# Optimization experiments

Measured on AMD Instinct MI355X. Metric: run time of the kernel, lower is better.

Reference implementation:

```python
import jax, jax.numpy as jnp
import numpy as np

I = 128   # input_size
H = 256   # state_size


def setup_inputs() -> dict:
    key = jax.random.key(0)
    ks = jax.random.split(key, 7)
    T, B = 512, 1024
    # Xavier-ish init scales for params
    s_ih = 1.0 / np.sqrt(I)
    s_hh = 1.0 / np.sqrt(H)
    return {
        "x":    jax.random.normal(ks[0], (T, B, I), dtype=jnp.float32),
        "W_ih": jax.random.normal(ks[1], (4 * H, I), dtype=jnp.float32) * s_ih,
        "W_hh": jax.random.normal(ks[2], (4 * H, H), dtype=jnp.float32) * s_hh,
        "b_ih": jax.random.normal(ks[3], (4 * H,), dtype=jnp.float32) * s_hh,
        "b_hh": jax.random.normal(ks[4], (4 * H,), dtype=jnp.float32) * s_hh,
        "hx0":  jax.random.normal(ks[5], (H,), dtype=jnp.float32) * s_hh,
        "cx0":  jax.random.normal(ks[6], (H,), dtype=jnp.float32) * s_hh,
    }


def _lstm_forward(x, W_ih, W_hh, b_ih, b_hh, hx0, cx0):
    T, B, _ = x.shape
    past_length = T - 1  # use_last_past=False
    x_used = x[:past_length]
    # Precompute input projections for all steps at once: [T-1, B, 4H]
    x_proj = jnp.einsum("tbi,gi->tbg", x_used, W_ih) + b_ih + b_hh

    h0 = jnp.broadcast_to(hx0, (B, H))
    c0 = jnp.broadcast_to(cx0, (B, H))

    def step(carry, xp):
        h, c = carry
        gates = xp + h @ W_hh.T  # [B, 4H]
        i_g, f_g, g_g, o_g = jnp.split(gates, 4, axis=-1)
        i_g = jax.nn.sigmoid(i_g)
        f_g = jax.nn.sigmoid(f_g)
        g_g = jnp.tanh(g_g)
        o_g = jax.nn.sigmoid(o_g)
        c_new = f_g * c + i_g * g_g
        h_new = o_g * jnp.tanh(c_new)
        return (h_new, c_new), None

    (h, c), _ = jax.lax.scan(step, (h0, c0), x_proj)
    return h, c


def reference(x, W_ih, W_hh, b_ih, b_hh, hx0, cx0):
    return _lstm_forward(x, W_ih, W_hh, b_ih, b_hh, hx0, cx0)
```

## Files before the change

kernel.cpp:

```cpp
#include <hip/hip_runtime.h>
#include <hip/hip_bf16.h>


#define T_STEPS 511
#define BATCH   1024
#define IN      128
#define HID     256
#define NG      1024
#define KTOT    384
#define BWG     16
#define NGROUP  64
#define SW      264
#define HS      264

typedef __bf16 bf16x8 __attribute__((ext_vector_type(8)));
typedef float  f32x4  __attribute__((ext_vector_type(4)));
typedef unsigned long long u64;

#define WCAT_OFF 0
#define BIAS_OFF 786432
#define HEXG_OFF 790528
#define CNT_OFF  1839104

__global__ void precast_kernel(const float* __restrict__ W_ih,
                               const float* __restrict__ W_hh,
                               const float* __restrict__ b_ih,
                               const float* __restrict__ b_hh,
                               __bf16* __restrict__ wcat,
                               float* __restrict__ bias,
                               int* __restrict__ cnt) {
    int idx = blockIdx.x * blockDim.x + threadIdx.x;
    if (idx < NG * KTOT) {
        int n = idx / KTOT, k = idx % KTOT;
        float v = (k < IN) ? W_ih[n * IN + k] : W_hh[n * HID + (k - IN)];
        wcat[idx] = (__bf16)v;
    }
    if (idx < NG) bias[idx] = b_ih[idx] + b_hh[idx];
    if (idx < NGROUP * 32) cnt[idx] = 0;
}

__device__ __forceinline__ float sigmoidf_fast(float v) {
    return 1.f / (1.f + __expf(-v));
}
__device__ __forceinline__ float tanhf_fast(float v) {
    return 1.f - 2.f / (1.f + __expf(2.f * v));
}

#define MFMA(a, b, c) __builtin_amdgcn_mfma_f32_16x16x32_bf16((a), (b), (c), 0, 0, 0)

__device__ __forceinline__ bf16x8 cvt_pack(float4 lo, float4 hi) {
    return bf16x8{(__bf16)lo.x, (__bf16)lo.y, (__bf16)lo.z, (__bf16)lo.w,
                  (__bf16)hi.x, (__bf16)hi.y, (__bf16)hi.z, (__bf16)hi.w};
}

__global__ __launch_bounds__(512, 2) void lstm_kernel(
    const float* __restrict__ x,
    const __bf16* __restrict__ wcat,
    const float* __restrict__ bias,
    const float* __restrict__ hx0,
    const float* __restrict__ cx0,
    __bf16* __restrict__ hexg,
    int* __restrict__ cnt,
    float* __restrict__ out)
{
    __shared__ alignas(16) __bf16 Whh[256 * SW];
    __shared__ alignas(16) __bf16 Ah[BWG * HS];

    const int tid  = threadIdx.x;
    const int bx   = blockIdx.x;
    const int g    = bx & 63;
    const int s    = bx >> 6;
    const int wave = tid >> 6;
    const int lane = tid & 63;
    const int col  = lane & 15;
    const int quad = lane >> 4;
    const int hf   = col >> 3;
    const int b0   = g * BWG;
    const int j0   = s * 64;
    const int jcol = j0 + wave * 8 + (col & 7);

    int* cntg = cnt + g * 32;

    {
        int r  = tid >> 1;
        int hh = (tid & 1) * 128;
        int ngl = ((r >> 6) << 8) + j0 + (r & 63);
        const __bf16* src = wcat + (size_t)ngl * KTOT + IN + hh;
        __bf16* dst = &Whh[r * SW + hh];
        #pragma unroll
        for (int i = 0; i < 16; ++i)
            *(bf16x8*)(dst + i * 8) = *(const bf16x8*)(src + i * 8);
    }

    const int n0 = (hf ? 256 : 0) + jcol;
    const int n1 = 512 + (hf ? 256 : 0) + jcol;
    bf16x8 wi0[4], wi1[4];
    #pragma unroll
    for (int ks = 0; ks < 4; ++ks) {
        wi0[ks] = *(const bf16x8*)(wcat + (size_t)n0 * KTOT + ks * 32 + quad * 8);
        wi1[ks] = *(const bf16x8*)(wcat + (size_t)n1 * KTOT + ks * 32 + quad * 8);
    }

    const float bi  = bias[jcol];
    const float bfv = bias[256 + jcol];
    const float bg  = bias[512 + jcol];
    const float bo  = bias[768 + jcol];

    float cst[4], hn[4];
    {
        float cv = cx0[jcol];
        #pragma unroll
        for (int r = 0; r < 4; ++r) cst[r] = cv;
    }

    float4 x0f[8], xf[8];
    #pragma unroll
    for (int ks = 0; ks < 4; ++ks) {
        const float* xp = x + (size_t)(b0 + col) * IN + ks * 32 + quad * 8;
        x0f[2 * ks]     = *(const float4*)xp;
        x0f[2 * ks + 1] = *(const float4*)(xp + 4);
        const float* xq = xp + (size_t)BATCH * IN;
        xf[2 * ks]      = *(const float4*)xq;
        xf[2 * ks + 1]  = *(const float4*)(xq + 4);
    }

    const int nl0 = hf * 64 + wave * 8 + (col & 7);
    const __bf16* wl0 = &Whh[nl0 * SW + quad * 8];
    const __bf16* wl1 = &Whh[(128 + nl0) * SW + quad * 8];

    __syncthreads();

    f32x4 aA0 = {0.f,0.f,0.f,0.f}, aA1 = {0.f,0.f,0.f,0.f};
    f32x4 aB0 = {0.f,0.f,0.f,0.f}, aB1 = {0.f,0.f,0.f,0.f};
    {
        bf16x8 ax[4];
        #pragma unroll
        for (int ks = 0; ks < 4; ++ks)
            ax[ks] = cvt_pack(x0f[2 * ks], x0f[2 * ks + 1]);
        aA0 = MFMA(ax[0], wi0[0], aA0); aB0 = MFMA(ax[0], wi1[0], aB0);
        aA1 = MFMA(ax[1], wi0[1], aA1); aB1 = MFMA(ax[1], wi1[1], aB1);
        aA0 = MFMA(ax[2], wi0[2], aA0); aB0 = MFMA(ax[2], wi1[2], aB0);
        aA1 = MFMA(ax[3], wi0[3], aA1); aB1 = MFMA(ax[3], wi1[3], aB1);
    }

    for (int t = 0; t < T_STEPS; ++t) {
        bf16x8 ahf[8];
        if (t == 0) {
            #pragma unroll
            for (int ks = 0; ks < 8; ++ks) {
                const float* hp = hx0 + ks * 32 + quad * 8;
                ahf[ks] = cvt_pack(*(const float4*)hp, *(const float4*)(hp + 4));
            }
        } else {
            const int target = 32 * t;
            int guard = 0;
            while (__hip_atomic_load(cntg, __ATOMIC_RELAXED,
                                     __HIP_MEMORY_SCOPE_AGENT) < target) {
                __builtin_amdgcn_s_sleep(1);
                if (++guard > (1 << 22)) break;
            }
            const u64* sp = (const u64*)(hexg
                + ((size_t)((t & 1) * NGROUP + g)) * (BWG * HID)) + tid * 2;
            u64 v0 = __hip_atomic_load(sp,     __ATOMIC_RELAXED, __HIP_MEMORY_SCOPE_AGENT);
            u64 v1 = __hip_atomic_load(sp + 1, __ATOMIC_RELAXED, __HIP_MEMORY_SCOPE_AGENT);
            int row = tid >> 5, c8 = (tid & 31) * 8;
            *(u64*)&Ah[row * HS + c8]     = v0;
            *(u64*)&Ah[row * HS + c8 + 4] = v1;
            __syncthreads();
            #pragma unroll
            for (int ks = 0; ks < 8; ++ks)
                ahf[ks] = *(const bf16x8*)&Ah[col * HS + ks * 32 + quad * 8];
        }

        #pragma unroll
        for (int ks = 0; ks < 4; ++ks) {
            bf16x8 w0a = *(const bf16x8*)(wl0 + ks * 32);
            bf16x8 w1a = *(const bf16x8*)(wl1 + ks * 32);
            bf16x8 w0b = *(const bf16x8*)(wl0 + (ks + 4) * 32);
            bf16x8 w1b = *(const bf16x8*)(wl1 + (ks + 4) * 32);
            aA0 = MFMA(ahf[ks],     w0a, aA0);
            aB0 = MFMA(ahf[ks],     w1a, aB0);
            aA1 = MFMA(ahf[ks + 4], w0b, aA1);
            aB1 = MFMA(ahf[ks + 4], w1b, aB1);
        }
        f32x4 accA = aA0 + aA1;
        f32x4 accB = aB0 + aB1;

        #pragma unroll
        for (int r = 0; r < 4; ++r) {
            float oA = __shfl_xor(accA[r], 8, 64);
            float oB = __shfl_xor(accB[r], 8, 64);
            float iv = (hf ? oA : accA[r]) + bi;
            float fv = (hf ? accA[r] : oA) + bfv;
            float gv = (hf ? oB : accB[r]) + bg;
            float ov = (hf ? accB[r] : oB) + bo;
            float ig = sigmoidf_fast(iv);
            float fg = sigmoidf_fast(fv);
            float gt = tanhf_fast(gv);
            float og = sigmoidf_fast(ov);
            float cn = fg * cst[r] + ig * gt;
            cst[r] = cn;
            hn[r]  = og * tanhf_fast(cn);
        }

        if (t < T_STEPS - 1) {
            __bf16* base = hexg
                + ((size_t)((((t + 1) & 1) * NGROUP) + g)) * (BWG * HID);
            #pragma unroll
            for (int r = 0; r < 4; ++r) {
                unsigned short mine;
                {
                    __bf16 hv = (__bf16)hn[r];
                    __builtin_memcpy(&mine, &hv, 2);
                }
                int other = __shfl_xor((int)mine, 1, 64);
                if ((col & 1) == 0 && col < 8) {
                    unsigned int val = (unsigned int)mine
                                     | ((unsigned int)(unsigned short)other << 16);
                    unsigned int* p = (unsigned int*)(base
                        + (size_t)(quad * 4 + r) * HID + jcol);
                    __hip_atomic_store(p, val, __ATOMIC_RELAXED,
                                       __HIP_MEMORY_SCOPE_AGENT);
                }
            }
            asm volatile("s_waitcnt vmcnt(0)" ::: "memory");
            if (lane == 0)
                __hip_atomic_fetch_add(cntg, 1, __ATOMIC_RELAXED,
                                       __HIP_MEMORY_SCOPE_AGENT);

            {
                bf16x8 ax[4];
                #pragma unroll
                for (int ks = 0; ks < 4; ++ks)
                    ax[ks] = cvt_pack(xf[2 * ks], xf[2 * ks + 1]);
                aA0 = {0.f,0.f,0.f,0.f}; aA1 = {0.f,0.f,0.f,0.f};
                aB0 = {0.f,0.f,0.f,0.f}; aB1 = {0.f,0.f,0.f,0.f};
                aA0 = MFMA(ax[0], wi0[0], aA0); aB0 = MFMA(ax[0], wi1[0], aB0);
                aA1 = MFMA(ax[1], wi0[1], aA1); aB1 = MFMA(ax[1], wi1[1], aB1);
                aA0 = MFMA(ax[2], wi0[2], aA0); aB0 = MFMA(ax[2], wi1[2], aB0);
                aA1 = MFMA(ax[3], wi0[3], aA1); aB1 = MFMA(ax[3], wi1[3], aB1);
            }
            if (t + 2 <= T_STEPS - 1) {
                #pragma unroll
                for (int ks = 0; ks < 4; ++ks) {
                    const float* xp = x + (size_t)(t + 2) * BATCH * IN
                                    + (size_t)(b0 + col) * IN + ks * 32 + quad * 8;
                    xf[2 * ks]     = *(const float4*)xp;
                    xf[2 * ks + 1] = *(const float4*)(xp + 4);
                }
            }
        }
    }

    if (col < 8) {
        #pragma unroll
        for (int r = 0; r < 4; ++r) {
            int row = b0 + quad * 4 + r;
            out[(size_t)row * HID + jcol] = hn[r];
            out[(size_t)BATCH * HID + (size_t)row * HID + jcol] = cst[r];
        }
    }
}

extern "C" void kernel_launch(void* const* d_in, const int* in_sizes, int n_in,
                              void* d_out, int out_size, void* d_ws, size_t ws_size,
                              hipStream_t stream) {
    const float* x    = (const float*)d_in[0];
    const float* W_ih = (const float*)d_in[1];
    const float* W_hh = (const float*)d_in[2];
    const float* b_ih = (const float*)d_in[3];
    const float* b_hh = (const float*)d_in[4];
    const float* hx0  = (const float*)d_in[5];
    const float* cx0  = (const float*)d_in[6];
    float* outp = (float*)d_out;

    __bf16* wcat = (__bf16*)((char*)d_ws + WCAT_OFF);
    float*  bias = (float*)((char*)d_ws + BIAS_OFF);
    __bf16* hexg = (__bf16*)((char*)d_ws + HEXG_OFF);
    int*    cnt  = (int*)((char*)d_ws + CNT_OFF);

    precast_kernel<<<dim3((NG * KTOT + 255) / 256), dim3(256), 0, stream>>>(
        W_ih, W_hh, b_ih, b_hh, wcat, bias, cnt);

    void* args[] = {(void*)&x, (void*)&wcat, (void*)&bias, (void*)&hx0,
                    (void*)&cx0, (void*)&hexg, (void*)&cnt, (void*)&outp};
    hipLaunchCooperativeKernel((const void*)lstm_kernel, dim3(256), dim3(512),
                               args, 0, stream);
}
```

Baseline: 2.983 ms.

## Keep W_hh in registers, replace LDS staging and atomic counter with per-wave flags

Moves each lane's slice of W_hh from shared memory into registers, removing the per-step LDS weight reads. Each lane now reads its hidden-state MFMA fragment directly from global memory with coherent (sc0 sc1) loads, which removes the LDS staging buffer and the per-step __syncthreads. The atomic fetch_add counter is replaced by per-wave 16-bit step flags that every wave polls across 32 flags with __all. The wave-level waits should cut per-step latency on the serial recurrence, but they add register pressure, more global traffic, and a much shorter spin guard.

```diff
diff --git a/kernel.cpp b/kernel.cpp
--- a/kernel.cpp
+++ b/kernel.cpp
@@ -10,11 +10,10 @@
 #define KTOT    384
 #define BWG     16
 #define NGROUP  64
-#define SW      264
-#define HS      264
 
 typedef __bf16 bf16x8 __attribute__((ext_vector_type(8)));
 typedef float  f32x4  __attribute__((ext_vector_type(4)));
+typedef unsigned int u32x4 __attribute__((ext_vector_type(4)));
 typedef unsigned long long u64;
 
 #define WCAT_OFF 0
@@ -53,6 +52,48 @@
                   (__bf16)hi.x, (__bf16)hi.y, (__bf16)hi.z, (__bf16)hi.w};
 }
 
+
+__device__ __forceinline__ unsigned ld_u16_coh(const unsigned short* p) {
+    unsigned v;
+    asm volatile("global_load_ushort %0, %1, off sc0 sc1\n\t"
+                 "s_waitcnt vmcnt(0)"
+                 : "=&v"(v) : "v"(p) : "memory");
+    return v;
+}
+
+__device__ __forceinline__ void st_u32_coh(unsigned* p, unsigned v) {
+    asm volatile("global_store_dword %0, %1, off sc0 sc1" :: "v"(p), "v"(v) : "memory");
+}
+
+__device__ __forceinline__ void st_u16_coh(unsigned short* p, unsigned v) {
+    asm volatile("global_store_short %0, %1, off sc0 sc1" :: "v"(p), "v"(v) : "memory");
+}
+
+__device__ __forceinline__ void ld_hfrag(bf16x8 (&a)[8], const __bf16* base) {
+    u32x4 t0, t1, t2, t3, t4, t5, t6, t7;
+    asm volatile(
+        "global_load_dwordx4 %0, %8, off sc0 sc1\n\t"
+        "global_load_dwordx4 %1, %8, off offset:64 sc0 sc1\n\t"
+        "global_load_dwordx4 %2, %8, off offset:128 sc0 sc1\n\t"
+        "global_load_dwordx4 %3, %8, off offset:192 sc0 sc1\n\t"
+        "global_load_dwordx4 %4, %8, off offset:256 sc0 sc1\n\t"
+        "global_load_dwordx4 %5, %8, off offset:320 sc0 sc1\n\t"
+        "global_load_dwordx4 %6, %8, off offset:384 sc0 sc1\n\t"
+        "global_load_dwordx4 %7, %8, off offset:448 sc0 sc1\n\t"
+        "s_waitcnt vmcnt(0)"
+        : "=&v"(t0), "=&v"(t1), "=&v"(t2), "=&v"(t3),
+          "=&v"(t4), "=&v"(t5), "=&v"(t6), "=&v"(t7)
+        : "v"(base) : "memory");
+    a[0] = __builtin_bit_cast(bf16x8, t0);
+    a[1] = __builtin_bit_cast(bf16x8, t1);
+    a[2] = __builtin_bit_cast(bf16x8, t2);
+    a[3] = __builtin_bit_cast(bf16x8, t3);
+    a[4] = __builtin_bit_cast(bf16x8, t4);
+    a[5] = __builtin_bit_cast(bf16x8, t5);
+    a[6] = __builtin_bit_cast(bf16x8, t6);
+    a[7] = __builtin_bit_cast(bf16x8, t7);
+}
+
 __global__ __launch_bounds__(512, 2) void lstm_kernel(
     const float* __restrict__ x,
     const __bf16* __restrict__ wcat,
@@ -63,9 +104,6 @@
     int* __restrict__ cnt,
     float* __restrict__ out)
 {
-    __shared__ alignas(16) __bf16 Whh[256 * SW];
-    __shared__ alignas(16) __bf16 Ah[BWG * HS];
-
     const int tid  = threadIdx.x;
     const int bx   = blockIdx.x;
     const int g    = bx & 63;
@@ -79,26 +117,20 @@
     const int j0   = s * 64;
     const int jcol = j0 + wave * 8 + (col & 7);
 
-    int* cntg = cnt + g * 32;
-
-    {
-        int r  = tid >> 1;
-        int hh = (tid & 1) * 128;
-        int ngl = ((r >> 6) << 8) + j0 + (r & 63);
-        const __bf16* src = wcat + (size_t)ngl * KTOT + IN + hh;
-        __bf16* dst = &Whh[r * SW + hh];
-        #pragma unroll
-        for (int i = 0; i < 16; ++i)
-            *(bf16x8*)(dst + i * 8) = *(const bf16x8*)(src + i * 8);
-    }
+    unsigned short* flags = (unsigned short*)cnt;
 
     const int n0 = (hf ? 256 : 0) + jcol;
     const int n1 = 512 + (hf ? 256 : 0) + jcol;
-    bf16x8 wi0[4], wi1[4];
+    bf16x8 wi0[4], wi1[4], wh0[8], wh1[8];
     #pragma unroll
     for (int ks = 0; ks < 4; ++ks) {
         wi0[ks] = *(const bf16x8*)(wcat + (size_t)n0 * KTOT + ks * 32 + quad * 8);
         wi1[ks] = *(const bf16x8*)(wcat + (size_t)n1 * KTOT + ks * 32 + quad * 8);
+    }
+    #pragma unroll
+    for (int ks = 0; ks < 8; ++ks) {
+        wh0[ks] = *(const bf16x8*)(wcat + (size_t)n0 * KTOT + IN + ks * 32 + quad * 8);
+        wh1[ks] = *(const bf16x8*)(wcat + (size_t)n1 * KTOT + IN + ks * 32 + quad * 8);
     }
 
     const float bi  = bias[jcol];
@@ -124,11 +156,16 @@
         xf[2 * ks + 1]  = *(const float4*)(xq + 4);
     }
 
-    const int nl0 = hf * 64 + wave * 8 + (col & 7);
-    const __bf16* wl0 = &Whh[nl0 * SW + quad * 8];
-    const __bf16* wl1 = &Whh[(128 + nl0) * SW + quad * 8];
-
-    __syncthreads();
+    const __bf16* hb0 = hexg + (size_t)g * (BWG * HID) + col * HID + quad * 8;
+    const __bf16* hb1 = hb0 + (size_t)NGROUP * (BWG * HID);
+    unsigned *pb0, *pb1;
+    {
+        __bf16* pp = hexg + (size_t)g * (BWG * HID) + (size_t)(quad * 4) * HID + jcol;
+        pb0 = (unsigned*)pp;
+        pb1 = (unsigned*)(pp + (size_t)NGROUP * (BWG * HID));
+    }
+    const unsigned short* fpoll = flags + g * 32 + (lane & 31);
+    unsigned short*       fmine = flags + g * 32 + s * 8 + wave;
 
     f32x4 aA0 = {0.f,0.f,0.f,0.f}, aA1 = {0.f,0.f,0.f,0.f};
     f32x4 aB0 = {0.f,0.f,0.f,0.f}, aB1 = {0.f,0.f,0.f,0.f};
@@ -152,36 +189,23 @@
                 ahf[ks] = cvt_pack(*(const float4*)hp, *(const float4*)(hp + 4));
             }
         } else {
-            const int target = 32 * t;
             int guard = 0;
-            while (__hip_atomic_load(cntg, __ATOMIC_RELAXED,
-                                     __HIP_MEMORY_SCOPE_AGENT) < target) {
+            for (;;) {
+                unsigned fv = ld_u16_coh(fpoll);
+                if (__all((int)fv >= t)) break;
+                if (++guard > (1 << 16)) break;
                 __builtin_amdgcn_s_sleep(1);
-                if (++guard > (1 << 22)) break;
-            }
-            const u64* sp = (const u64*)(hexg
-                + ((size_t)((t & 1) * NGROUP + g)) * (BWG * HID)) + tid * 2;
-            u64 v0 = __hip_atomic_load(sp,     __ATOMIC_RELAXED, __HIP_MEMORY_SCOPE_AGENT);
-            u64 v1 = __hip_atomic_load(sp + 1, __ATOMIC_RELAXED, __HIP_MEMORY_SCOPE_AGENT);
-            int row = tid >> 5, c8 = (tid & 31) * 8;
-            *(u64*)&Ah[row * HS + c8]     = v0;
-            *(u64*)&Ah[row * HS + c8 + 4] = v1;
-            __syncthreads();
-            #pragma unroll
-            for (int ks = 0; ks < 8; ++ks)
-                ahf[ks] = *(const bf16x8*)&Ah[col * HS + ks * 32 + quad * 8];
+            }
+            const __bf16* hbase = (t & 1) ? hb1 : hb0;
+            ld_hfrag(ahf, hbase);
         }
 
         #pragma unroll
         for (int ks = 0; ks < 4; ++ks) {
-            bf16x8 w0a = *(const bf16x8*)(wl0 + ks * 32);
-            bf16x8 w1a = *(const bf16x8*)(wl1 + ks * 32);
-            bf16x8 w0b = *(const bf16x8*)(wl0 + (ks + 4) * 32);
-            bf16x8 w1b = *(const bf16x8*)(wl1 + (ks + 4) * 32);
-            aA0 = MFMA(ahf[ks],     w0a, aA0);
-            aB0 = MFMA(ahf[ks],     w1a, aB0);
-            aA1 = MFMA(ahf[ks + 4], w0b, aA1);
-            aB1 = MFMA(ahf[ks + 4], w1b, aB1);
+            aA0 = MFMA(ahf[ks],     wh0[ks],     aA0);
+            aB0 = MFMA(ahf[ks],     wh1[ks],     aB0);
+            aA1 = MFMA(ahf[ks + 4], wh0[ks + 4], aA1);
+            aB1 = MFMA(ahf[ks + 4], wh1[ks + 4], aB1);
         }
         f32x4 accA = aA0 + aA1;
         f32x4 accB = aB0 + aB1;
@@ -204,8 +228,7 @@
         }
 
         if (t < T_STEPS - 1) {
-            __bf16* base = hexg
-                + ((size_t)((((t + 1) & 1) * NGROUP) + g)) * (BWG * HID);
+            unsigned* pb = (t & 1) ? pb0 : pb1;
             #pragma unroll
             for (int r = 0; r < 4; ++r) {
                 unsigned short mine;
@@ -215,18 +238,13 @@
                 }
                 int other = __shfl_xor((int)mine, 1, 64);
                 if ((col & 1) == 0 && col < 8) {
-                    unsigned int val = (unsigned int)mine
-                                     | ((unsigned int)(unsigned short)other << 16);
-                    unsigned int* p = (unsigned int*)(base
-                        + (size_t)(quad * 4 + r) * HID + jcol);
-                    __hip_atomic_store(p, val, __ATOMIC_RELAXED,
-                                       __HIP_MEMORY_SCOPE_AGENT);
+                    unsigned val = (unsigned)mine
+                                 | ((unsigned)(unsigned short)other << 16);
+                    st_u32_coh(pb + r * 128, val);
                 }
             }
             asm volatile("s_waitcnt vmcnt(0)" ::: "memory");
-            if (lane == 0)
-                __hip_atomic_fetch_add(cntg, 1, __ATOMIC_RELAXED,
-                                       __HIP_MEMORY_SCOPE_AGENT);
+            if (lane == 0) st_u16_coh(fmine, (unsigned)(t + 1));
 
             {
                 bf16x8 ax[4];
```

Result: slower. 4.261 ms (+42.8%).
